# Kernel tuning notes

Measured on AMD Instinct MI355X. Metric: run time of the kernel, lower is better.

The kernel has to match this reference:

```python
import jax, jax.numpy as jnp
import numpy as np

B, T, C = 4, 2048, 1024
NH = 16
HD = C // NH


def setup_inputs() -> dict:
    key = jax.random.key(0)
    ks = jax.random.split(key, 5)
    s = 0.02
    return {
        "x": jax.random.normal(ks[0], (B, T, C), dtype=jnp.float32),
        "w_attn": jax.random.normal(ks[1], (C, 3 * C), dtype=jnp.float32) * s,
        "b_attn": jnp.zeros((3 * C,), dtype=jnp.float32),
        "w_proj": jax.random.normal(ks[2], (C, C), dtype=jnp.float32) * s,
        "b_proj": jnp.zeros((C,), dtype=jnp.float32),
    }


def reference(x, w_attn, b_attn, w_proj, b_proj):
    Bx, Tx, Cx = x.shape
    qkv = x @ w_attn + b_attn                       # [B,T,3C]
    q, k, v = jnp.split(qkv, 3, axis=-1)
    # [B,T,C] -> [B,NH,T,HD]
    def heads(t):
        return t.reshape(Bx, Tx, NH, HD).transpose(0, 2, 1, 3)
    q, k, v = heads(q), heads(k), heads(v)
    scale = HD ** -0.5
    attn = jnp.einsum("bhqd,bhkd->bhqk", q, k) * scale
    causal = jnp.tril(jnp.ones((Tx, Tx), dtype=bool))
    attn = jnp.where(causal[None, None], attn, -jnp.inf)
    attn = jax.nn.softmax(attn, axis=-1)
    out = jnp.einsum("bhqk,bhkd->bhqd", attn, v)    # [B,NH,T,HD]
    out = out.transpose(0, 2, 1, 3).reshape(Bx, Tx, Cx)
    return out @ w_proj + b_proj
```

## Files before the change

### kernel.cpp

```cpp
#include <hip/hip_runtime.h>
#include <hip/hip_bf16.h>
#include <stdint.h>

using f32x4  = __attribute__((ext_vector_type(4))) float;
using bf16x8 = __attribute__((ext_vector_type(8))) short;
using u16x4  = __attribute__((ext_vector_type(4))) ushort;

#define MFMA16(a, b, c) __builtin_amdgcn_mfma_f32_16x16x32_bf16((a), (b), (c), 0, 0, 0)

__device__ __forceinline__ void gload_lds16(const void* g, void* l) {
    __builtin_amdgcn_global_load_lds(
        (const __attribute__((address_space(1))) void*)g,
        (__attribute__((address_space(3))) void*)l, 16, 0, 0);
}

__device__ __forceinline__ ushort f2bf(float f) {
    union { float f; uint32_t u; } v; v.f = f;
    uint32_t r = v.u + 0x7fffu + ((v.u >> 16) & 1u);
    return (ushort)(r >> 16);
}
__device__ __forceinline__ float bf2f(ushort u) {
    union { uint32_t u; float f; } v; v.u = ((uint32_t)u) << 16;
    return v.f;
}
__device__ __forceinline__ uint32_t pk_bf16(float a, float b) {
    __hip_bfloat162 h = __float22bfloat162_rn(float2{a, b});
    union { __hip_bfloat162 h; uint32_t u; } v; v.h = h; return v.u;
}
__device__ __forceinline__ bf16x8 scale8(bf16x8 v, float s) {
    bf16x8 r;
#pragma unroll
    for (int j = 0; j < 8; ++j) r[j] = (short)f2bf(bf2f((ushort)v[j]) * s);
    return r;
}

__device__ __forceinline__ void wgbar() {
    asm volatile("" ::: "memory");
    __builtin_amdgcn_s_barrier();
    asm volatile("" ::: "memory");
}
#define VMW8 asm volatile("s_waitcnt vmcnt(8)" ::: "memory")
#define VMW0 asm volatile("s_waitcnt vmcnt(0)" ::: "memory")

#define NEG_BIG (-1.0e30f)

__global__ void pack_bf16_k(const float* __restrict__ in, ushort* __restrict__ out, int n4) {
    const int i = blockIdx.x * blockDim.x + threadIdx.x;
    if (i >= n4) return;
    const f32x4 v = *(const f32x4*)(in + (size_t)i * 4);
    u16x4 o;
    o[0] = f2bf(v[0]); o[1] = f2bf(v[1]); o[2] = f2bf(v[2]); o[3] = f2bf(v[3]);
    *(u16x4*)(out + (size_t)i * 4) = o;
}

__global__ void transpose_k(const float* __restrict__ in, ushort* __restrict__ out,
                            int R, int C) {
    __shared__ ushort tile[32][33];
    const int c0 = blockIdx.x * 32, r0 = blockIdx.y * 32;
    const int tx = threadIdx.x, ty = threadIdx.y;
    for (int i = ty; i < 32; i += 8)
        tile[i][tx] = f2bf(in[(size_t)(r0 + i) * C + c0 + tx]);
    __syncthreads();
    for (int i = ty; i < 32; i += 8)
        out[(size_t)(c0 + i) * R + r0 + tx] = tile[tx][i];
}

template <int MODE>
__global__ __launch_bounds__(512, 2)
void gemm256(const ushort* __restrict__ A, const ushort* __restrict__ BT,
             const float* __restrict__ bias, float* __restrict__ outF,
             ushort* __restrict__ qk, ushort* __restrict__ vt,
             int N, int K) {
    __shared__ __align__(16) ushort As[2][256 * 64];
    __shared__ __align__(16) ushort Bs[2][256 * 64];
    const int tid  = threadIdx.x;
    const int lane = tid & 63;
    const int wid  = tid >> 6;
    const int l15  = lane & 15, lg = lane >> 4;
    const int wm = (wid >> 2) * 128;
    const int wn = (wid & 3) * 64;

    const int cpx = gridDim.x >> 3;
    const int swz = (blockIdx.x & 7) * cpx + (blockIdx.x >> 3);
    const int tile_m = (swz & 31) << 8;
    const int tile_n = (swz >> 5) << 8;

    const f32x4 fzero = {0.f, 0.f, 0.f, 0.f};
    f32x4 acc[8][4];
#pragma unroll
    for (int i = 0; i < 8; ++i)
#pragma unroll
        for (int j = 0; j < 4; ++j) acc[i][j] = fzero;

    const ushort* aP[4]; const ushort* bP[4]; int dOff[4];
#pragma unroll
    for (int i = 0; i < 4; ++i) {
        const int c = i * 512 + tid;
        const int row = c >> 3;
        const int ch = (c & 7) ^ (row & 7);
        aP[i] = A  + (size_t)(tile_m + row) * K + ch * 8;
        bP[i] = BT + (size_t)(tile_n + row) * K + ch * 8;
        dOff[i] = c * 16;
    }

    auto STAGE = [&](int buf, int kt) {
        const int k0 = kt * 64;
#pragma unroll
        for (int i = 0; i < 4; ++i) gload_lds16(aP[i] + k0, (char*)As[buf] + dOff[i]);
#pragma unroll
        for (int i = 0; i < 4; ++i) gload_lds16(bP[i] + k0, (char*)Bs[buf] + dOff[i]);
    };

    auto COMPUTE = [&](int buf) {
        const char* Ab = (const char*)As[buf];
        const char* Bb = (const char*)Bs[buf];
#pragma unroll
        for (int kk = 0; kk < 2; ++kk) {
            bf16x8 a[8], b[4];
#pragma unroll
            for (int mf = 0; mf < 8; ++mf) {
                const int row = wm + mf * 16 + l15;
                a[mf] = *(const bf16x8*)(Ab + row * 128 + ((((kk << 2) + lg) ^ (row & 7)) << 4));
            }
#pragma unroll
            for (int nf = 0; nf < 4; ++nf) {
                const int row = wn + nf * 16 + l15;
                b[nf] = *(const bf16x8*)(Bb + row * 128 + ((((kk << 2) + lg) ^ (row & 7)) << 4));
            }
#pragma unroll
            for (int mf = 0; mf < 8; ++mf)
#pragma unroll
                for (int nf = 0; nf < 4; ++nf)
                    acc[mf][nf] = MFMA16(a[mf], b[nf], acc[mf][nf]);
        }
    };

    const int nt = K >> 6;
    STAGE(0, 0);
    STAGE(1, 1);
    int cur = 0;
    for (int t = 0; t < nt; ++t) {
        if (t < nt - 1) { VMW8; } else { VMW0; }
        wgbar();
        COMPUTE(cur);
        wgbar();
        if (t + 2 < nt) STAGE(cur, t + 2);
        cur ^= 1;
    }

#pragma unroll
    for (int nf = 0; nf < 4; ++nf) {
        const int col = tile_n + wn + nf * 16 + l15;
        const float bv = bias[col];
#pragma unroll
        for (int mf = 0; mf < 8; ++mf) {
            const int row = tile_m + wm + mf * 16 + lg * 4;
            float v0 = acc[mf][nf][0] + bv, v1 = acc[mf][nf][1] + bv;
            float v2 = acc[mf][nf][2] + bv, v3 = acc[mf][nf][3] + bv;
            if (MODE == 0) {
                outF[(size_t)(row + 0) * N + col] = v0;
                outF[(size_t)(row + 1) * N + col] = v1;
                outF[(size_t)(row + 2) * N + col] = v2;
                outF[(size_t)(row + 3) * N + col] = v3;
            } else {
                if (col < 2048) {
                    qk[(size_t)(row + 0) * 2048 + col] = f2bf(v0);
                    qk[(size_t)(row + 1) * 2048 + col] = f2bf(v1);
                    qk[(size_t)(row + 2) * 2048 + col] = f2bf(v2);
                    qk[(size_t)(row + 3) * 2048 + col] = f2bf(v3);
                } else {
                    const int vc = col - 2048;
                    const int bb = row >> 11, t = row & 2047;
                    uint2 w; w.x = pk_bf16(v0, v1); w.y = pk_bf16(v2, v3);
                    *(uint2*)(vt + ((size_t)(bb * 16 + (vc >> 6)) * 64 + (vc & 63)) * 2048 + t) = w;
                }
            }
        }
    }
}

__global__ __launch_bounds__(256)
void attn_fwd(const ushort* __restrict__ qk, const ushort* __restrict__ vt,
              ushort* __restrict__ ao) {
    const int tid  = threadIdx.x;
    const int lane = tid & 63;
    const int w    = tid >> 6;
    const int l15  = lane & 15, lg = lane >> 4;
    const int bh = blockIdx.y;
    const int b = bh >> 4, h = bh & 15;

    __shared__ __align__(16) ushort Ks[2][64 * 64];
    __shared__ __align__(16) ushort Vs[2][64 * 64];
    __shared__ __align__(16) ushort Ps[4][32 * 80];

    char* psw = (char*)&Ps[w][0];
    const int pswz = (l15 & 7) << 4;

    const ushort* kbase = qk + (size_t)b * 2048 * 2048 + 1024 + h * 64;
    const ushort* vbase = vt + (size_t)bh * 64 * 2048;
    const float sscale = 0.125f * 1.4426950408889634f;

    const int srow0 = tid >> 3,         schk0 = (tid & 7) ^ (srow0 & 7);
    const int srow1 = (256 + tid) >> 3, schk1 = (tid & 7) ^ (srow1 & 7);

    for (int pass = 0; pass < 2; ++pass) {
        const int q0 = (pass ? (15 - blockIdx.x) : blockIdx.x) * 128;
        const int qw = q0 + w * 32;

        const ushort* qrow = qk + ((size_t)(b * 2048 + qw + l15)) * 2048 + h * 64 + lg * 8;
        bf16x8 qf[2][2];
        qf[0][0] = scale8(*(const bf16x8*)(qrow), sscale);
        qf[0][1] = scale8(*(const bf16x8*)(qrow + 32), sscale);
        qf[1][0] = scale8(*(const bf16x8*)(qrow + 16 * 2048), sscale);
        qf[1][1] = scale8(*(const bf16x8*)(qrow + 16 * 2048 + 32), sscale);

        const f32x4 fzero = {0.f, 0.f, 0.f, 0.f};
        f32x4 o[2][4];
#pragma unroll
        for (int qh = 0; qh < 2; ++qh)
#pragma unroll
            for (int f = 0; f < 4; ++f) o[qh][f] = fzero;
        float mrun[2] = {NEG_BIG, NEG_BIG};
        float lrun[2] = {0.f, 0.f};

        const int nt = q0 / 64 + 2;

        {
            gload_lds16(kbase + (size_t)srow0 * 2048 + schk0 * 8, (char*)Ks[0] + tid * 16);
            gload_lds16(kbase + (size_t)srow1 * 2048 + schk1 * 8, (char*)Ks[0] + (256 + tid) * 16);
            gload_lds16(vbase + (size_t)srow0 * 2048 + schk0 * 8, (char*)Vs[0] + tid * 16);
            gload_lds16(vbase + (size_t)srow1 * 2048 + schk1 * 8, (char*)Vs[0] + (256 + tid) * 16);
        }
        __syncthreads();

        for (int t = 0; t < nt; ++t) {
            const int cur = t & 1;
            const int kv0 = t * 64;
            if (t + 1 < nt) {
                const int nkv = kv0 + 64;
                ushort* kd = Ks[cur ^ 1];
                ushort* vd = Vs[cur ^ 1];
                gload_lds16(kbase + (size_t)(nkv + srow0) * 2048 + schk0 * 8, (char*)kd + tid * 16);
                gload_lds16(kbase + (size_t)(nkv + srow1) * 2048 + schk1 * 8, (char*)kd + (256 + tid) * 16);
                gload_lds16(vbase + (size_t)srow0 * 2048 + nkv + schk0 * 8, (char*)vd + tid * 16);
                gload_lds16(vbase + (size_t)srow1 * 2048 + nkv + schk1 * 8, (char*)vd + (256 + tid) * 16);
            }

            if (kv0 <= qw + 31) {
                const char* kls = (const char*)Ks[cur];
                const char* vls = (const char*)Vs[cur];

                bf16x8 kf[4][2];
#pragma unroll
                for (int hh = 0; hh < 4; ++hh)
#pragma unroll
                    for (int dc = 0; dc < 2; ++dc)
                        kf[hh][dc] = *(const bf16x8*)(kls + (hh * 16 + l15) * 128 +
                                                      (((dc * 4 + lg) ^ (l15 & 7)) << 4));

#pragma unroll
                for (int qh = 0; qh < 2; ++qh) {
                    if (kv0 > qw + qh * 16 + 15) continue;
                    f32x4 st[4] = {fzero, fzero, fzero, fzero};
#pragma unroll
                    for (int hh = 0; hh < 4; ++hh)
#pragma unroll
                        for (int dc = 0; dc < 2; ++dc)
                            st[hh] = MFMA16(kf[hh][dc], qf[qh][dc], st[hh]);

                    float p[16];
#pragma unroll
                    for (int hh = 0; hh < 4; ++hh)
#pragma unroll
                        for (int i = 0; i < 4; ++i) p[hh * 4 + i] = st[hh][i];
                    if (kv0 + 63 > qw + qh * 16) {
                        const int qg = qw + qh * 16 + l15;
#pragma unroll
                        for (int hh = 0; hh < 4; ++hh)
#pragma unroll
                            for (int i = 0; i < 4; ++i) {
                                const int kvg = kv0 + hh * 16 + lg * 4 + i;
                                if (kvg > qg) p[hh * 4 + i] = NEG_BIG;
                            }
                    }

                    float mt = p[0];
#pragma unroll
                    for (int j = 1; j < 16; ++j) mt = fmaxf(mt, p[j]);
                    mt = fmaxf(mt, __shfl_xor(mt, 16));
                    mt = fmaxf(mt, __shfl_xor(mt, 32));

                    if (!__all(mt <= mrun[qh])) {
                        const float mn = fmaxf(mrun[qh], mt);
                        const float alpha = exp2f(mrun[qh] - mn);
                        mrun[qh] = mn;
                        float ar[4];
#pragma unroll
                        for (int i = 0; i < 4; ++i) ar[i] = __shfl(alpha, lg * 4 + i);
#pragma unroll
                        for (int f = 0; f < 4; ++f)
#pragma unroll
                            for (int i = 0; i < 4; ++i) o[qh][f][i] *= ar[i];
                        lrun[qh] *= alpha;
                    }

                    float rs = 0.f;
#pragma unroll
                    for (int j = 0; j < 16; ++j) { p[j] = exp2f(p[j] - mrun[qh]); rs += p[j]; }
                    rs += __shfl_xor(rs, 16);
                    rs += __shfl_xor(rs, 32);
                    lrun[qh] += rs;

                    const int prow = qh * 16 + l15;
#pragma unroll
                    for (int hh = 0; hh < 4; ++hh) {
                        uint2 pk;
                        pk.x = pk_bf16(p[hh * 4 + 0], p[hh * 4 + 1]);
                        pk.y = pk_bf16(p[hh * 4 + 2], p[hh * 4 + 3]);
                        *(uint2*)(psw + ((prow * 160 + hh * 32 + lg * 8) ^ pswz)) = pk;
                    }
                }

                bf16x8 pf[2][2];
#pragma unroll
                for (int qh = 0; qh < 2; ++qh)
#pragma unroll
                    for (int ks = 0; ks < 2; ++ks)
                        pf[qh][ks] = *(const bf16x8*)(psw + (((qh * 16 + l15) * 160 + ks * 64 + lg * 16) ^ pswz));

#pragma unroll
                for (int f = 0; f < 4; ++f) {
                    const int vrow = f * 16 + l15;
                    bf16x8 vf0 = *(const bf16x8*)(vls + vrow * 128 + ((lg ^ (l15 & 7)) << 4));
                    bf16x8 vf1 = *(const bf16x8*)(vls + vrow * 128 + (((4 + lg) ^ (l15 & 7)) << 4));
#pragma unroll
                    for (int qh = 0; qh < 2; ++qh) {
                        if (kv0 > qw + qh * 16 + 15) continue;
                        o[qh][f] = MFMA16(pf[qh][0], vf0, o[qh][f]);
                        o[qh][f] = MFMA16(pf[qh][1], vf1, o[qh][f]);
                    }
                }
            }
            __syncthreads();
        }

#pragma unroll
        for (int qh = 0; qh < 2; ++qh) {
            float lr[4];
#pragma unroll
            for (int i = 0; i < 4; ++i) lr[i] = __shfl(lrun[qh], lg * 4 + i);
#pragma unroll
            for (int f = 0; f < 4; ++f)
#pragma unroll
                for (int i = 0; i < 4; ++i) {
                    const int row = qw + qh * 16 + lg * 4 + i;
                    const int col = h * 64 + f * 16 + l15;
                    ao[((size_t)(b * 2048 + row)) * 1024 + col] = f2bf(o[qh][f][i] / lr[i]);
                }
        }
    }
}

extern "C" void kernel_launch(void* const* d_in, const int* in_sizes, int n_in,
                              void* d_out, int out_size, void* d_ws, size_t ws_size,
                              hipStream_t stream) {
    const float* x      = (const float*)d_in[0];
    const float* w_attn = (const float*)d_in[1];
    const float* b_attn = (const float*)d_in[2];
    const float* w_proj = (const float*)d_in[3];
    const float* b_proj = (const float*)d_in[4];
    float* out = (float*)d_out;

    ushort* ws  = (ushort*)d_ws;
    ushort* xb  = ws;
    ushort* wTa = xb  + (size_t)8192 * 1024;
    ushort* wTp = wTa + (size_t)3072 * 1024;
    ushort* qkb = wTp + (size_t)1024 * 1024;
    ushort* vtb = qkb + (size_t)8192 * 2048;
    ushort* aob = vtb + (size_t)64 * 64 * 2048;
    const size_t needed = ((size_t)8192 * 1024 + (size_t)3072 * 1024 + (size_t)1024 * 1024 +
                           (size_t)8192 * 2048 + (size_t)64 * 64 * 2048 + (size_t)8192 * 1024) * 2;
    if (ws_size < needed) return;

    pack_bf16_k<<<8192, 256, 0, stream>>>(x, xb, 8192 * 1024 / 4);
    transpose_k<<<dim3(96, 32), dim3(32, 8), 0, stream>>>(w_attn, wTa, 1024, 3072);
    transpose_k<<<dim3(32, 32), dim3(32, 8), 0, stream>>>(w_proj, wTp, 1024, 1024);
    gemm256<1><<<384, 512, 0, stream>>>(xb, wTa, b_attn, nullptr, qkb, vtb, 3072, 1024);
    attn_fwd<<<dim3(8, 64), 256, 0, stream>>>(qkb, vtb, aob);
    gemm256<0><<<128, 512, 0, stream>>>(aob, wTp, b_proj, out, nullptr, nullptr, 1024, 1024);
}
```

Before: 330.3 us.

## Split GEMM main loop into quadrant phases with interleaved prefetch and setprio

The bf16 GEMM k-loop now runs in four quadrant phases. Each phase loads a half of the A or B fragments from LDS, waits on lgkmcnt, and runs its MFMA block at raised wave priority (s_setprio). The global-to-LDS prefetch for stage t+2 is split into separate A and B halves, issued between phases once the matching LDS data has been consumed. The goal is to overlap LDS reads, global loads and MFMA work across waves in a ping-pong style. The cost is more workgroup barriers per iteration, which could stall waves if the phases do not balance.

```diff
diff --git a/kernel.cpp b/kernel.cpp
--- a/kernel.cpp
+++ b/kernel.cpp
@@ -39,8 +39,11 @@
     __builtin_amdgcn_s_barrier();
     asm volatile("" ::: "memory");
 }
-#define VMW8 asm volatile("s_waitcnt vmcnt(8)" ::: "memory")
-#define VMW0 asm volatile("s_waitcnt vmcnt(0)" ::: "memory")
+#define VMW8  asm volatile("s_waitcnt vmcnt(8)" ::: "memory")
+#define VMW0  asm volatile("s_waitcnt vmcnt(0)" ::: "memory")
+#define LGK0  asm volatile("s_waitcnt lgkmcnt(0)" ::: "memory")
+#define PRIO1 __builtin_amdgcn_s_setprio(1)
+#define PRIO0 __builtin_amdgcn_s_setprio(0)
 
 #define NEG_BIG (-1.0e30f)
 
@@ -92,59 +95,78 @@
 #pragma unroll
         for (int j = 0; j < 4; ++j) acc[i][j] = fzero;
 
-    const ushort* aP[4]; const ushort* bP[4]; int dOff[4];
-#pragma unroll
-    for (int i = 0; i < 4; ++i) {
-        const int c = i * 512 + tid;
-        const int row = c >> 3;
-        const int ch = (c & 7) ^ (row & 7);
-        aP[i] = A  + (size_t)(tile_m + row) * K + ch * 8;
-        bP[i] = BT + (size_t)(tile_n + row) * K + ch * 8;
-        dOff[i] = c * 16;
-    }
-
-    auto STAGE = [&](int buf, int kt) {
-        const int k0 = kt * 64;
-#pragma unroll
-        for (int i = 0; i < 4; ++i) gload_lds16(aP[i] + k0, (char*)As[buf] + dOff[i]);
-#pragma unroll
-        for (int i = 0; i < 4; ++i) gload_lds16(bP[i] + k0, (char*)Bs[buf] + dOff[i]);
+    const int srow = tid >> 3;
+    const int sch  = (tid & 7) ^ (srow & 7);
+    const ushort* aP0 = A  + (size_t)(tile_m + srow) * K + sch * 8;
+    const ushort* bP0 = BT + (size_t)(tile_n + srow) * K + sch * 8;
+    const int d0 = tid * 16;
+
+    auto STA = [&](int buf, int kt) {
+#pragma unroll
+        for (int i = 0; i < 4; ++i)
+            gload_lds16(aP0 + (size_t)i * 64 * K + kt * 64, (char*)As[buf] + d0 + i * 8192);
     };
-
-    auto COMPUTE = [&](int buf) {
-        const char* Ab = (const char*)As[buf];
-        const char* Bb = (const char*)Bs[buf];
-#pragma unroll
-        for (int kk = 0; kk < 2; ++kk) {
-            bf16x8 a[8], b[4];
-#pragma unroll
-            for (int mf = 0; mf < 8; ++mf) {
-                const int row = wm + mf * 16 + l15;
-                a[mf] = *(const bf16x8*)(Ab + row * 128 + ((((kk << 2) + lg) ^ (row & 7)) << 4));
-            }
-#pragma unroll
-            for (int nf = 0; nf < 4; ++nf) {
-                const int row = wn + nf * 16 + l15;
-                b[nf] = *(const bf16x8*)(Bb + row * 128 + ((((kk << 2) + lg) ^ (row & 7)) << 4));
-            }
-#pragma unroll
-            for (int mf = 0; mf < 8; ++mf)
-#pragma unroll
-                for (int nf = 0; nf < 4; ++nf)
-                    acc[mf][nf] = MFMA16(a[mf], b[nf], acc[mf][nf]);
-        }
+    auto STB = [&](int buf, int kt) {
+#pragma unroll
+        for (int i = 0; i < 4; ++i)
+            gload_lds16(bP0 + (size_t)i * 64 * K + kt * 64, (char*)Bs[buf] + d0 + i * 8192);
     };
+    auto LDA = [&](const char* Ab, int mh, bf16x8* ar) {
+#pragma unroll
+        for (int mf = 0; mf < 4; ++mf) {
+            const int row = wm + (mh * 4 + mf) * 16 + l15;
+#pragma unroll
+            for (int kk = 0; kk < 2; ++kk)
+                ar[mf * 2 + kk] = *(const bf16x8*)(Ab + row * 128 + ((((kk << 2) + lg) ^ (row & 7)) << 4));
+        }
+    };
+    auto LDB = [&](const char* Bb, int nh, bf16x8* br) {
+#pragma unroll
+        for (int nf = 0; nf < 2; ++nf) {
+            const int row = wn + (nh * 2 + nf) * 16 + l15;
+#pragma unroll
+            for (int kk = 0; kk < 2; ++kk)
+                br[nf * 2 + kk] = *(const bf16x8*)(Bb + row * 128 + ((((kk << 2) + lg) ^ (row & 7)) << 4));
+        }
+    };
+    auto MM = [&](const bf16x8* ar, const bf16x8* br, int mh, int nh) {
+#pragma unroll
+        for (int mf = 0; mf < 4; ++mf)
+#pragma unroll
+            for (int nf = 0; nf < 2; ++nf)
+#pragma unroll
+                for (int kk = 0; kk < 2; ++kk)
+                    acc[mh * 4 + mf][nh * 2 + nf] =
+                        MFMA16(ar[mf * 2 + kk], br[nf * 2 + kk], acc[mh * 4 + mf][nh * 2 + nf]);
+    };
 
     const int nt = K >> 6;
-    STAGE(0, 0);
-    STAGE(1, 1);
+    STA(0, 0); STB(0, 0);
+    STA(1, 1); STB(1, 1);
     int cur = 0;
     for (int t = 0; t < nt; ++t) {
+        const char* Ab = (const char*)As[cur];
+        const char* Bb = (const char*)Bs[cur];
+        const bool pre = (t + 2 < nt);
         if (t < nt - 1) { VMW8; } else { VMW0; }
         wgbar();
-        COMPUTE(cur);
+        bf16x8 ar[8], br01[4], br23[4];
+        LDA(Ab, 0, ar); LDB(Bb, 0, br01);
+        wgbar(); LGK0;
+        PRIO1; MM(ar, br01, 0, 0); PRIO0;
         wgbar();
-        if (t + 2 < nt) STAGE(cur, t + 2);
+        LDB(Bb, 1, br23);
+        wgbar(); LGK0;
+        PRIO1; MM(ar, br23, 0, 1); PRIO0;
+        wgbar();
+        LDA(Ab, 1, ar);
+        if (pre) STB(cur, t + 2);
+        wgbar(); LGK0;
+        PRIO1; MM(ar, br23, 1, 1); PRIO0;
+        wgbar();
+        if (pre) STA(cur, t + 2);
+        __builtin_amdgcn_sched_barrier(0);
+        PRIO1; MM(ar, br01, 1, 0); PRIO0;
         cur ^= 1;
     }
 
@@ -170,9 +192,9 @@
                     qk[(size_t)(row + 3) * 2048 + col] = f2bf(v3);
                 } else {
                     const int vc = col - 2048;
-                    const int bb = row >> 11, t = row & 2047;
+                    const int bb = row >> 11, tt = row & 2047;
                     uint2 w; w.x = pk_bf16(v0, v1); w.y = pk_bf16(v2, v3);
-                    *(uint2*)(vt + ((size_t)(bb * 16 + (vc >> 6)) * 64 + (vc & 63)) * 2048 + t) = w;
+                    *(uint2*)(vt + ((size_t)(bb * 16 + (vc >> 6)) * 64 + (vc & 63)) * 2048 + tt) = w;
                 }
             }
         }
```

New measurement: 326.6 us. Within noise of the previous version (-1.1%).
